# Kernel optimization log

Hardware: AMD Instinct MI355X
Metric: run time of the kernel (lower is better)

The kernel has to match this reference:

```python
import jax, jax.numpy as jnp
import numpy as np

HID = 1024            # hidden_dim
COND = 80             # cond_dim (mel bins)
EMB = HID // 8        # 128
D = HID // 4          # 256
NC = 2 ** 8           # num_coarse_bits = 8
NF = 2 ** 8           # num_fine_bits = 8
N, L = 32, 1024


def _vs(key, shape):
    # VarianceScaling(1.0, fan_in, truncated_normal) approximated by normal/sqrt(fan_in)
    return jax.random.normal(key, shape, jnp.float32) / jnp.sqrt(jnp.float32(shape[0]))


def setup_inputs() -> dict:
    key = jax.random.key(0)
    ks = jax.random.split(key, 16)
    x = jax.random.randint(ks[0], (N, L, 2), 0, NC, dtype=jnp.int64)
    mel = jax.random.normal(ks[1], (N, L, COND), jnp.float32)
    return {
        "x": x,
        "mel": mel,
        "R_w": _vs(ks[2], (HID, 3 * HID)),
        "R_b": jnp.zeros((3 * HID,), jnp.float32),
        "I_W": _vs(ks[3], (COND + 3 * EMB, 3 * HID)),
        "I_b": jnp.zeros((1, 3 * HID), jnp.float32),
        "O1_w": _vs(ks[4], (3 * D, 3 * D)),
        "O1_b": jnp.zeros((3 * D,), jnp.float32),
        "O2_w": _vs(ks[5], (3 * D, NC)),
        "O2_b": jnp.zeros((NC,), jnp.float32),
        "O3_w": _vs(ks[6], (D, D)),
        "O3_b": jnp.zeros((D,), jnp.float32),
        "O4_w": _vs(ks[7], (D, NF)),
        "O4_b": jnp.zeros((NF,), jnp.float32),
        "c_emb": jax.random.normal(ks[8], (NC, EMB), jnp.float32) * 0.02,
        "f_emb": jax.random.normal(ks[9], (NF, EMB), jnp.float32) * 0.02,
    }


def _mask_like(I_W):
    # zero out future-coarse embedding rows for the coarse-prediction gate halves
    m = jnp.ones_like(I_W)
    m = m.at[-EMB:, 0 * D:3 * D].set(0.0)
    m = m.at[-EMB:, 4 * D:7 * D].set(0.0)
    m = m.at[-EMB:, 8 * D:11 * D].set(0.0)
    return m


def _forward(x, mel, R_w, R_b, I_W, I_b, O1_w, O1_b, O2_w, O2_b, O3_w, O3_b, O4_w, O4_b, c_emb, f_emb):
    c = x[..., 0]
    f = x[..., 1]
    c_next = jnp.roll(c, -1, -1)
    # [N, L, COND + 3*EMB]
    inp = jnp.concatenate((mel, c_emb[c], f_emb[f], c_emb[c_next]), axis=-1)
    IW = I_W * _mask_like(I_W)
    # input projection is time-independent -> precompute for all steps: [N, L, 3H]
    xproj = jnp.einsum("nld,dh->nlh", inp, IW) + I_b[0]

    def step(h, xt):
        u1, r1, e1 = jnp.split(h @ R_w + R_b, 3, axis=-1)
        u2, r2, e2 = jnp.split(xt, 3, axis=-1)
        u = jax.nn.sigmoid(u1 + u2)
        r = jax.nn.sigmoid(r1 + r2)
        e = jnp.tanh(r * e1 + e2)
        h = u * h + (1.0 - u) * e
        return h, h

    h0 = jnp.zeros((x.shape[0], HID), xproj.dtype)
    _, hs = jax.lax.scan(step, h0, jnp.swapaxes(xproj, 0, 1))  # [L, N, H]
    hs = jnp.swapaxes(hs, 0, 1)                                 # [N, L, H]
    yc = hs[..., : 3 * D]
    yf = hs[..., 3 * D:]
    clogits = jax.nn.relu(yc @ O1_w + O1_b) @ O2_w + O2_b
    flogits = jax.nn.relu(yf @ O3_w + O3_b) @ O4_w + O4_b
    return clogits, flogits


def reference(x, mel, R_w, R_b, I_W, I_b, O1_w, O1_b, O2_w, O2_b, O3_w, O3_b, O4_w, O4_b, c_emb, f_emb):
    return _forward(x, mel, R_w, R_b, I_W, I_b, O1_w, O1_b, O2_w, O2_b,
                    O3_w, O3_b, O4_w, O4_b, c_emb, f_emb)
```

## Files before the change

### kernel.cpp

```cpp
#include <hip/hip_runtime.h>
#include <hip/hip_bf16.h>
#include <math.h>

typedef __attribute__((ext_vector_type(4))) float vf4;
typedef __attribute__((ext_vector_type(8))) short vbf8;
typedef __attribute__((ext_vector_type(8))) unsigned short vus8;

#define NWG   128
#define NTHR  256
#define LEN   1024
#define H3    3072
#define CND   80
#define EMBD  128

#define TAB1_B  0ull
#define TAB2_B  (TAB1_B + 786432ull*4)
#define TAB3_B  (TAB2_B + 786432ull*4)
#define BF_B    (TAB3_B + 786432ull*4)
#define MELA_B  (BF_B   + 4587520ull*2)
#define AF_B    (MELA_B + 3145728ull*2)
#define CNT_B   (AF_B   + 33587200ull*2)
#define W1F_B   (CNT_B + 4096ull)
#define W2F_B   (W1F_B + 1179648ull)
#define W3F_B   (W2F_B + 393216ull)
#define W4F_B   (W3F_B + 131072ull)
#define FOFS    8388608ull


__global__ __launch_bounds__(256) void make_tables(const float* __restrict__ IW,
                                                   const float* __restrict__ Ib,
                                                   const float* __restrict__ cemb,
                                                   const float* __restrict__ femb,
                                                   float* __restrict__ tab1,
                                                   float* __restrict__ tab2,
                                                   float* __restrict__ tab3) {
    int blk = blockIdx.x;
    int table = blk / 3072;
    int rem = blk % 3072;
    int row = rem / 12;
    int cc = rem % 12;
    int col = cc * 256 + threadIdx.x;
    int ofs = CND + table * EMBD;
    const float* emb = (table == 1) ? femb : cemb;
    float acc = 0.f;
    for (int k = 0; k < EMBD; ++k)
        acc += emb[row * EMBD + k] * IW[(size_t)(ofs + k) * H3 + col];
    if (table == 0) acc += Ib[col];
    if (table == 2 && ((col & 1023) < 768)) acc = 0.f;
    float* dst = (table == 0) ? tab1 : (table == 1 ? tab2 : tab3);
    dst[(size_t)row * H3 + col] = acc;
}

__global__ __launch_bounds__(256) void build_bfrag2(const float* __restrict__ Rw,
                                                    const float* __restrict__ IW,
                                                    const float* __restrict__ Rb,
                                                    unsigned short* __restrict__ Bf) {
    int idx = blockIdx.x * 256 + threadIdx.x;
    int col = idx % 3072;
    int k   = idx / 3072;
    float v;
    if (k < 1024)       v = Rw[(size_t)k * H3 + col];
    else if (k < 1104)  v = IW[(size_t)(k - 1024) * H3 + col];
    else if (k == 1104) v = Rb[col];
    else return;

    int g  = col >> 10;
    int j  = col & 1023;
    int oct = j >> 3, jo = j & 7;
    int which, c;
    if (g < 2)      { which = 0; c = g * 8 + jo; }
    else {
        which = 1;
        if (k < 1024 || k == 1104) c = jo;
        else                        c = 8 + jo;
    }
    int kk = k >> 5, r5 = k & 31;
    int lane = (r5 >> 3) * 16 + c;
    int elem = r5 & 7;
    size_t dst = (((size_t)oct * 2 + which) * 35 + kk) * 512 + lane * 8 + elem;
    __hip_bfloat16 hb = __float2bfloat16(v);
    Bf[dst] = *(unsigned short*)&hb;
}

__global__ __launch_bounds__(256) void build_melA(const float* __restrict__ mel,
                                                  unsigned short* __restrict__ MelA) {
    long idx = (long)blockIdx.x * 256 + threadIdx.x;
    int elem = idx & 7;
    int lane = (idx >> 3) & 63;
    int kkm  = (int)((idx >> 9) % 3);
    int m    = (int)((idx / 1536) & 1);
    int t    = (int)(idx / 3072);
    int b    = m * 16 + (lane & 15);
    int km   = kkm * 32 + ((lane >> 4) & 3) * 8 + elem;
    float v = (km < CND) ? mel[((size_t)b * LEN + t) * CND + km] : (km == CND ? 1.f : 0.f);
    __hip_bfloat16 hb = __float2bfloat16(v);
    MelA[idx] = *(unsigned short*)&hb;
}

__global__ __launch_bounds__(256) void build_wfrag(const float* __restrict__ W,
                                                   unsigned short* __restrict__ Wf,
                                                   int K, int N) {
    int idx = blockIdx.x * 256 + threadIdx.x;
    if (idx >= K * N) return;
    int col = idx % N;
    int k   = idx / N;
    int nt = col >> 4, c = col & 15;
    int kf = k >> 5, k5 = k & 31;
    int lane = c + 16 * (k5 >> 3);
    int elem = k5 & 7;
    size_t dst = ((size_t)nt * (K >> 5) + kf) * 512 + (size_t)lane * 8 + elem;
    __hip_bfloat16 hb = __float2bfloat16(W[idx]);
    Wf[dst] = *(unsigned short*)&hb;
}

__device__ __forceinline__ int is_sent(unsigned long long q) {
    return ((unsigned)q == 0xFFFFFFFFu) || ((unsigned)(q >> 32) == 0xFFFFFFFFu);
}

__global__ __launch_bounds__(256, 1) void scan_persist(const unsigned short* __restrict__ Bf,
                                                       const unsigned short* __restrict__ MelA,
                                                       unsigned short* __restrict__ Af,
                                                       const float* __restrict__ tab1,
                                                       const float* __restrict__ tab2,
                                                       const float* __restrict__ tab3,
                                                       const int* __restrict__ xin) {
    __shared__ __align__(16) unsigned short hstage[32 * 512];
    __shared__ float ex[16][68];

    int tid = threadIdx.x;
    int wg  = blockIdx.x;
    int lane = tid & 63;
    int wv = tid >> 6;
    int bh = wg >> 6;
    int jg = wg & 63;
    int p  = wv >> 1;
    int which = wv & 1;
    int oct = jg * 2 + p;

    vbf8 Breg[35];
    {
        const unsigned short* Bp = Bf + (((size_t)oct * 2 + which) * 35) * 512 + lane * 8;
#pragma unroll
        for (int kk = 0; kk < 35; ++kk)
            Breg[kk] = *(const vbf8*)(Bp + kk * 512);
    }

    int bl = tid >> 4, gjl = tid & 15;
    int gb = bh * 16 + bl;
    int gj = jg * 16 + gjl;
    float hreg = 0.f;
    size_t wbase = (size_t)((bh * 32 + (gj >> 5)) * 512 +
                            (bl + 16 * ((gj >> 3) & 3)) * 8 + (gj & 7));

#pragma unroll 1
    for (int t = 0; t < LEN; ++t) {
        int ci = xin[(gb * LEN + t) * 2];
        int fi = xin[(gb * LEN + t) * 2 + 1];
        int cn = xin[(gb * LEN + ((t + 1) & (LEN - 1))) * 2];
        float t1u = tab1[(size_t)ci * H3 + gj];
        float t2u = tab2[(size_t)fi * H3 + gj];
        float t3u = tab3[(size_t)cn * H3 + gj];
        float t1r = tab1[(size_t)ci * H3 + 1024 + gj];
        float t2r = tab2[(size_t)fi * H3 + 1024 + gj];
        float t3r = tab3[(size_t)cn * H3 + 1024 + gj];
        float t1e = tab1[(size_t)ci * H3 + 2048 + gj];
        float t2e = tab2[(size_t)fi * H3 + 2048 + gj];
        float t3e = tab3[(size_t)cn * H3 + 2048 + gj];

        int f0 = wv * 8;
        const unsigned long long* bp =
            (const unsigned long long*)(Af + (size_t)t * 32768 +
                                        (size_t)(bh * 32 + f0) * 512) + lane * 2;
        unsigned long long q[16];
#pragma unroll
        for (int i = 0; i < 8; ++i) {
            q[2 * i]     = __hip_atomic_load(bp + i * 128,     __ATOMIC_RELAXED, __HIP_MEMORY_SCOPE_AGENT);
            q[2 * i + 1] = __hip_atomic_load(bp + i * 128 + 1, __ATOMIC_RELAXED, __HIP_MEMORY_SCOPE_AGENT);
        }
        for (;;) {
            int bad = 0;
#pragma unroll
            for (int i = 0; i < 16; ++i) bad |= is_sent(q[i]);
            if (!__any(bad)) break;
            __builtin_amdgcn_s_sleep(1);
#pragma unroll
            for (int i = 0; i < 8; ++i) {
                q[2 * i]     = __hip_atomic_load(bp + i * 128,     __ATOMIC_RELAXED, __HIP_MEMORY_SCOPE_AGENT);
                q[2 * i + 1] = __hip_atomic_load(bp + i * 128 + 1, __ATOMIC_RELAXED, __HIP_MEMORY_SCOPE_AGENT);
            }
        }
#pragma unroll
        for (int i = 0; i < 8; ++i) {
            union { unsigned long long qq[2]; vus8 v; } u;
            u.qq[0] = q[2 * i]; u.qq[1] = q[2 * i + 1];
            *(vus8*)(hstage + (size_t)(f0 + i) * 512 + lane * 8) = u.v;
        }
        __syncthreads();

        const unsigned short* Am = MelA + (size_t)t * 3072 + (size_t)(bh * 3) * 512 + lane * 8;
        vf4 acc0 = {0.f, 0.f, 0.f, 0.f}, acc1 = {0.f, 0.f, 0.f, 0.f};
#pragma unroll
        for (int kq = 0; kq < 3; ++kq) {
            vbf8 a = *(const vbf8*)(Am + kq * 512);
            acc0 = __builtin_amdgcn_mfma_f32_16x16x32_bf16(a, Breg[32 + kq], acc0, 0, 0, 0);
        }

        const unsigned short* Ah = hstage + lane * 8;
#pragma unroll
        for (int kk = 0; kk < 32; kk += 2) {
            vbf8 a0v = *(const vbf8*)(Ah + kk * 512);
            acc0 = __builtin_amdgcn_mfma_f32_16x16x32_bf16(a0v, Breg[kk], acc0, 0, 0, 0);
            vbf8 a1v = *(const vbf8*)(Ah + (kk + 1) * 512);
            acc1 = __builtin_amdgcn_mfma_f32_16x16x32_bf16(a1v, Breg[kk + 1], acc1, 0, 0, 0);
        }
        vf4 acc = acc0 + acc1;

#pragma unroll
        for (int r = 0; r < 4; ++r)
            ex[(lane >> 4) * 4 + r][wv * 16 + (lane & 15)] = acc[r];
        __syncthreads();

        int pp = gjl >> 3, jo = gjl & 7;
        float gu  = ex[bl][(pp * 2) * 16 + jo]          + t1u + t2u + t3u;
        float gr  = ex[bl][(pp * 2) * 16 + 8 + jo]      + t1r + t2r + t3r;
        float e1  = ex[bl][(pp * 2 + 1) * 16 + jo];
        float ge2 = ex[bl][(pp * 2 + 1) * 16 + 8 + jo]  + t1e + t2e + t3e;
        float u  = 1.f / (1.f + expf(-gu));
        float r_ = 1.f / (1.f + expf(-gr));
        float e  = tanhf(r_ * e1 + ge2);
        hreg = u * hreg + (1.f - u) * e;

        __hip_bfloat16 hb = __float2bfloat16(hreg);
        int myv = (int)(*(unsigned short*)&hb);
        int nbv = __shfl_xor(myv, 1);
        if ((tid & 1) == 0) {
            unsigned int pk = ((unsigned)myv & 0xffffu) | ((unsigned)nbv << 16);
            __hip_atomic_store((unsigned int*)(Af + (size_t)(t + 1) * 32768 + wbase), pk,
                               __ATOMIC_RELAXED, __HIP_MEMORY_SCOPE_AGENT);
        }
        __syncthreads();
    }
}

__global__ __launch_bounds__(512) void out_mlp_mfma(
        const unsigned short* __restrict__ Af,
        const unsigned short* __restrict__ W1f, const float* __restrict__ O1b,
        const unsigned short* __restrict__ W2f, const float* __restrict__ O2b,
        const unsigned short* __restrict__ W3f, const float* __restrict__ O3b,
        const unsigned short* __restrict__ W4f, const float* __restrict__ O4b,
        float* __restrict__ out) {
    __shared__ __align__(16) unsigned short Zc[2 * 24 * 512];
    __shared__ __align__(16) unsigned short Zf[2 * 8 * 512];

    int tid = threadIdx.x;
    int lane = tid & 63;
    int wv = tid >> 6;
    int m = wv >> 2;
    int q = wv & 3;
    int l = blockIdx.x;
    int c16 = lane & 15;
    int rowq = lane >> 4;

    const unsigned short* Abase = Af + (size_t)(l + 1) * 32768 +
                                  (size_t)(m * 32) * 512 + (size_t)lane * 8;

    {
        vf4 acc[12];
#pragma unroll
        for (int i = 0; i < 12; ++i) acc[i] = (vf4){0.f, 0.f, 0.f, 0.f};
        for (int kk = 0; kk < 24; ++kk) {
            vbf8 a = *(const vbf8*)(Abase + kk * 512);
#pragma unroll
            for (int i = 0; i < 12; ++i) {
                int nt = q * 12 + i;
                vbf8 b = *(const vbf8*)(W1f + ((size_t)nt * 24 + kk) * 512 + lane * 8);
                acc[i] = __builtin_amdgcn_mfma_f32_16x16x32_bf16(a, b, acc[i], 0, 0, 0);
            }
        }
#pragma unroll
        for (int i = 0; i < 12; ++i) {
            int nt = q * 12 + i;
            int col = nt * 16 + c16;
            float bias = O1b[col];
#pragma unroll
            for (int r = 0; r < 4; ++r) {
                float v = fmaxf(acc[i][r] + bias, 0.f);
                __hip_bfloat16 hb = __float2bfloat16(v);
                int my = (int)*(unsigned short*)&hb;
                int nb = __shfl_xor(my, 1);
                if ((lane & 1) == 0) {
                    unsigned pk = ((unsigned)my & 0xffffu) | ((unsigned)nb << 16);
                    int row = rowq * 4 + r;
                    int kk2 = col >> 5, k5 = col & 31;
                    int lp = row + 16 * (k5 >> 3);
                    int ep = k5 & 7;
                    *(unsigned*)&Zc[(size_t)(m * 24 + kk2) * 512 + lp * 8 + ep] = pk;
                }
            }
        }
    }
    __syncthreads();

    {
        vf4 acc[4];
#pragma unroll
        for (int i = 0; i < 4; ++i) acc[i] = (vf4){0.f, 0.f, 0.f, 0.f};
        for (int kk = 0; kk < 24; ++kk) {
            vbf8 a = *(const vbf8*)(Zc + (size_t)(m * 24 + kk) * 512 + lane * 8);
#pragma unroll
            for (int i = 0; i < 4; ++i) {
                int nt = q * 4 + i;
                vbf8 b = *(const vbf8*)(W2f + ((size_t)nt * 24 + kk) * 512 + lane * 8);
                acc[i] = __builtin_amdgcn_mfma_f32_16x16x32_bf16(a, b, acc[i], 0, 0, 0);
            }
        }
#pragma unroll
        for (int i = 0; i < 4; ++i) {
            int nt = q * 4 + i;
            int col = nt * 16 + c16;
            float bias = O2b[col];
#pragma unroll
            for (int r = 0; r < 4; ++r) {
                int nn = m * 16 + rowq * 4 + r;
                out[((size_t)nn * 1024 + l) * 256 + col] = acc[i][r] + bias;
            }
        }
    }

    {
        vf4 acc[4];
#pragma unroll
        for (int i = 0; i < 4; ++i) acc[i] = (vf4){0.f, 0.f, 0.f, 0.f};
        for (int kf = 0; kf < 8; ++kf) {
            vbf8 a = *(const vbf8*)(Abase + (24 + kf) * 512);
#pragma unroll
            for (int i = 0; i < 4; ++i) {
                int nt = q * 4 + i;
                vbf8 b = *(const vbf8*)(W3f + ((size_t)nt * 8 + kf) * 512 + lane * 8);
                acc[i] = __builtin_amdgcn_mfma_f32_16x16x32_bf16(a, b, acc[i], 0, 0, 0);
            }
        }
#pragma unroll
        for (int i = 0; i < 4; ++i) {
            int nt = q * 4 + i;
            int col = nt * 16 + c16;
            float bias = O3b[col];
#pragma unroll
            for (int r = 0; r < 4; ++r) {
                float v = fmaxf(acc[i][r] + bias, 0.f);
                __hip_bfloat16 hb = __float2bfloat16(v);
                int my = (int)*(unsigned short*)&hb;
                int nb = __shfl_xor(my, 1);
                if ((lane & 1) == 0) {
                    unsigned pk = ((unsigned)my & 0xffffu) | ((unsigned)nb << 16);
                    int row = rowq * 4 + r;
                    int kk2 = col >> 5, k5 = col & 31;
                    int lp = row + 16 * (k5 >> 3);
                    int ep = k5 & 7;
                    *(unsigned*)&Zf[(size_t)(m * 8 + kk2) * 512 + lp * 8 + ep] = pk;
                }
            }
        }
    }
    __syncthreads();

    {
        vf4 acc[4];
#pragma unroll
        for (int i = 0; i < 4; ++i) acc[i] = (vf4){0.f, 0.f, 0.f, 0.f};
        for (int kf = 0; kf < 8; ++kf) {
            vbf8 a = *(const vbf8*)(Zf + (size_t)(m * 8 + kf) * 512 + lane * 8);
#pragma unroll
            for (int i = 0; i < 4; ++i) {
                int nt = q * 4 + i;
                vbf8 b = *(const vbf8*)(W4f + ((size_t)nt * 8 + kf) * 512 + lane * 8);
                acc[i] = __builtin_amdgcn_mfma_f32_16x16x32_bf16(a, b, acc[i], 0, 0, 0);
            }
        }
#pragma unroll
        for (int i = 0; i < 4; ++i) {
            int nt = q * 4 + i;
            int col = nt * 16 + c16;
            float bias = O4b[col];
#pragma unroll
            for (int r = 0; r < 4; ++r) {
                int nn = m * 16 + rowq * 4 + r;
                out[FOFS + ((size_t)nn * 1024 + l) * 256 + col] = acc[i][r] + bias;
            }
        }
    }
}

extern "C" void kernel_launch(void* const* d_in, const int* in_sizes, int n_in,
                              void* d_out, int out_size, void* d_ws, size_t ws_size,
                              hipStream_t stream) {
    const int*   x    = (const int*)d_in[0];
    const float* mel  = (const float*)d_in[1];
    const float* Rw   = (const float*)d_in[2];
    const float* Rb   = (const float*)d_in[3];
    const float* IW   = (const float*)d_in[4];
    const float* Ib   = (const float*)d_in[5];
    const float* O1w  = (const float*)d_in[6];
    const float* O1b  = (const float*)d_in[7];
    const float* O2w  = (const float*)d_in[8];
    const float* O2b  = (const float*)d_in[9];
    const float* O3w  = (const float*)d_in[10];
    const float* O3b  = (const float*)d_in[11];
    const float* O4w  = (const float*)d_in[12];
    const float* O4b  = (const float*)d_in[13];
    const float* cemb = (const float*)d_in[14];
    const float* femb = (const float*)d_in[15];
    char* wsb = (char*)d_ws;
    float* out = (float*)d_out;

    float* tab1 = (float*)(wsb + TAB1_B);
    float* tab2 = (float*)(wsb + TAB2_B);
    float* tab3 = (float*)(wsb + TAB3_B);
    unsigned short* Bf   = (unsigned short*)(wsb + BF_B);
    unsigned short* MelA = (unsigned short*)(wsb + MELA_B);
    unsigned short* Af   = (unsigned short*)(wsb + AF_B);
    unsigned short* W1f  = (unsigned short*)(wsb + W1F_B);
    unsigned short* W2f  = (unsigned short*)(wsb + W2F_B);
    unsigned short* W3f  = (unsigned short*)(wsb + W3F_B);
    unsigned short* W4f  = (unsigned short*)(wsb + W4F_B);

    make_tables<<<9216, 256, 0, stream>>>(IW, Ib, cemb, femb, tab1, tab2, tab3);
    hipMemsetAsync((void*)Bf, 0, 4587520ull * 2, stream);
    build_bfrag2<<<13440, 256, 0, stream>>>(Rw, IW, Rb, Bf);
    build_melA<<<12288, 256, 0, stream>>>(mel, MelA);
    build_wfrag<<<2304, 256, 0, stream>>>(O1w, W1f, 768, 768);
    build_wfrag<<<768,  256, 0, stream>>>(O2w, W2f, 768, 256);
    build_wfrag<<<256,  256, 0, stream>>>(O3w, W3f, 256, 256);
    build_wfrag<<<256,  256, 0, stream>>>(O4w, W4f, 256, 256);
    hipMemsetAsync((void*)Af, 0xFF, 33587200ull * 2, stream);
    hipMemsetAsync((void*)Af, 0, 65536, stream);

    scan_persist<<<NWG, NTHR, 0, stream>>>(Bf, MelA, Af, tab1, tab2, tab3, x);

    out_mlp_mfma<<<1024, 512, 0, stream>>>(Af, W1f, O1b, W2f, O2b, W3f, O3b, W4f, O4b, out);
}
```

Measured before the change: 2.873 ms.

## Split recurrent matmul by K across waves and reduce partials in LDS

```diff
diff --git a/kernel.cpp b/kernel.cpp
--- a/kernel.cpp
+++ b/kernel.cpp
@@ -124,8 +124,7 @@
                                                        const float* __restrict__ tab2,
                                                        const float* __restrict__ tab3,
                                                        const int* __restrict__ xin) {
-    __shared__ __align__(16) unsigned short hstage[32 * 512];
-    __shared__ float ex[16][68];
+    __shared__ float pex[4][4][256];
 
     int tid = threadIdx.x;
     int wg  = blockIdx.x;
@@ -133,17 +132,11 @@
     int wv = tid >> 6;
     int bh = wg >> 6;
     int jg = wg & 63;
-    int p  = wv >> 1;
-    int which = wv & 1;
-    int oct = jg * 2 + p;
-
-    vbf8 Breg[35];
-    {
-        const unsigned short* Bp = Bf + (((size_t)oct * 2 + which) * 35) * 512 + lane * 8;
-#pragma unroll
-        for (int kk = 0; kk < 35; ++kk)
-            Breg[kk] = *(const vbf8*)(Bp + kk * 512);
-    }
+
+    const unsigned short* Bp0 = Bf + (((size_t)(jg * 2 + 0) * 2 + 0) * 35) * 512 + lane * 8;
+    const unsigned short* Bp1 = Bf + (((size_t)(jg * 2 + 0) * 2 + 1) * 35) * 512 + lane * 8;
+    const unsigned short* Bp2 = Bf + (((size_t)(jg * 2 + 1) * 2 + 0) * 35) * 512 + lane * 8;
+    const unsigned short* Bp3 = Bf + (((size_t)(jg * 2 + 1) * 2 + 1) * 35) * 512 + lane * 8;
 
     int bl = tid >> 4, gjl = tid & 15;
     int gb = bh * 16 + bl;
@@ -151,6 +144,10 @@
     float hreg = 0.f;
     size_t wbase = (size_t)((bh * 32 + (gj >> 5)) * 512 +
                             (bl + 16 * ((gj >> 3) & 3)) * 8 + (gj & 7));
+    int p  = gjl >> 3, jo = gjl & 7;
+    int nt_ur = p * 2, nt_e = p * 2 + 1;
+    int ru = ((bl >> 2) * 16 + jo) * 4 + (bl & 3);
+    int rr = ((bl >> 2) * 16 + 8 + jo) * 4 + (bl & 3);
 
 #pragma unroll 1
     for (int t = 0; t < LEN; ++t) {
@@ -167,10 +164,9 @@
         float t2e = tab2[(size_t)fi * H3 + 2048 + gj];
         float t3e = tab3[(size_t)cn * H3 + 2048 + gj];
 
-        int f0 = wv * 8;
         const unsigned long long* bp =
             (const unsigned long long*)(Af + (size_t)t * 32768 +
-                                        (size_t)(bh * 32 + f0) * 512) + lane * 2;
+                                        (size_t)(bh * 32 + wv * 8) * 512) + lane * 2;
         unsigned long long q[16];
 #pragma unroll
         for (int i = 0; i < 8; ++i) {
@@ -189,42 +185,41 @@
                 q[2 * i + 1] = __hip_atomic_load(bp + i * 128 + 1, __ATOMIC_RELAXED, __HIP_MEMORY_SCOPE_AGENT);
             }
         }
+
+        vf4 acc0 = {0.f, 0.f, 0.f, 0.f}, acc1 = {0.f, 0.f, 0.f, 0.f};
+        vf4 acc2 = {0.f, 0.f, 0.f, 0.f}, acc3 = {0.f, 0.f, 0.f, 0.f};
 #pragma unroll
         for (int i = 0; i < 8; ++i) {
-            union { unsigned long long qq[2]; vus8 v; } u;
-            u.qq[0] = q[2 * i]; u.qq[1] = q[2 * i + 1];
-            *(vus8*)(hstage + (size_t)(f0 + i) * 512 + lane * 8) = u.v;
-        }
+            union { unsigned long long qq[2]; vbf8 v; } ua;
+            ua.qq[0] = q[2 * i]; ua.qq[1] = q[2 * i + 1];
+            vbf8 a = ua.v;
+            int kk = wv * 8 + i;
+            acc0 = __builtin_amdgcn_mfma_f32_16x16x32_bf16(a, *(const vbf8*)(Bp0 + kk * 512), acc0, 0, 0, 0);
+            acc1 = __builtin_amdgcn_mfma_f32_16x16x32_bf16(a, *(const vbf8*)(Bp1 + kk * 512), acc1, 0, 0, 0);
+            acc2 = __builtin_amdgcn_mfma_f32_16x16x32_bf16(a, *(const vbf8*)(Bp2 + kk * 512), acc2, 0, 0, 0);
+            acc3 = __builtin_amdgcn_mfma_f32_16x16x32_bf16(a, *(const vbf8*)(Bp3 + kk * 512), acc3, 0, 0, 0);
+        }
+        if (wv < 3) {
+            vbf8 am = *(const vbf8*)(MelA + (size_t)t * 3072 + (size_t)(bh * 3 + wv) * 512 + lane * 8);
+            acc0 = __builtin_amdgcn_mfma_f32_16x16x32_bf16(am, *(const vbf8*)(Bp0 + (32 + wv) * 512), acc0, 0, 0, 0);
+            acc1 = __builtin_amdgcn_mfma_f32_16x16x32_bf16(am, *(const vbf8*)(Bp1 + (32 + wv) * 512), acc1, 0, 0, 0);
+            acc2 = __builtin_amdgcn_mfma_f32_16x16x32_bf16(am, *(const vbf8*)(Bp2 + (32 + wv) * 512), acc2, 0, 0, 0);
+            acc3 = __builtin_amdgcn_mfma_f32_16x16x32_bf16(am, *(const vbf8*)(Bp3 + (32 + wv) * 512), acc3, 0, 0, 0);
+        }
+
+        *(vf4*)&pex[wv][0][lane * 4] = acc0;
+        *(vf4*)&pex[wv][1][lane * 4] = acc1;
+        *(vf4*)&pex[wv][2][lane * 4] = acc2;
+        *(vf4*)&pex[wv][3][lane * 4] = acc3;
         __syncthreads();
 
-        const unsigned short* Am = MelA + (size_t)t * 3072 + (size_t)(bh * 3) * 512 + lane * 8;
-        vf4 acc0 = {0.f, 0.f, 0.f, 0.f}, acc1 = {0.f, 0.f, 0.f, 0.f};
-#pragma unroll
-        for (int kq = 0; kq < 3; ++kq) {
-            vbf8 a = *(const vbf8*)(Am + kq * 512);
-            acc0 = __builtin_amdgcn_mfma_f32_16x16x32_bf16(a, Breg[32 + kq], acc0, 0, 0, 0);
-        }
-
-        const unsigned short* Ah = hstage + lane * 8;
-#pragma unroll
-        for (int kk = 0; kk < 32; kk += 2) {
-            vbf8 a0v = *(const vbf8*)(Ah + kk * 512);
-            acc0 = __builtin_amdgcn_mfma_f32_16x16x32_bf16(a0v, Breg[kk], acc0, 0, 0, 0);
-            vbf8 a1v = *(const vbf8*)(Ah + (kk + 1) * 512);
-            acc1 = __builtin_amdgcn_mfma_f32_16x16x32_bf16(a1v, Breg[kk + 1], acc1, 0, 0, 0);
-        }
-        vf4 acc = acc0 + acc1;
-
-#pragma unroll
-        for (int r = 0; r < 4; ++r)
-            ex[(lane >> 4) * 4 + r][wv * 16 + (lane & 15)] = acc[r];
-        __syncthreads();
-
-        int pp = gjl >> 3, jo = gjl & 7;
-        float gu  = ex[bl][(pp * 2) * 16 + jo]          + t1u + t2u + t3u;
-        float gr  = ex[bl][(pp * 2) * 16 + 8 + jo]      + t1r + t2r + t3r;
-        float e1  = ex[bl][(pp * 2 + 1) * 16 + jo];
-        float ge2 = ex[bl][(pp * 2 + 1) * 16 + 8 + jo]  + t1e + t2e + t3e;
+        float gu  = pex[0][nt_ur][ru] + pex[1][nt_ur][ru] + pex[2][nt_ur][ru] + pex[3][nt_ur][ru]
+                  + t1u + t2u + t3u;
+        float gr  = pex[0][nt_ur][rr] + pex[1][nt_ur][rr] + pex[2][nt_ur][rr] + pex[3][nt_ur][rr]
+                  + t1r + t2r + t3r;
+        float e1  = pex[0][nt_e][ru] + pex[1][nt_e][ru] + pex[2][nt_e][ru] + pex[3][nt_e][ru];
+        float ge2 = pex[0][nt_e][rr] + pex[1][nt_e][rr] + pex[2][nt_e][rr] + pex[3][nt_e][rr]
+                  + t1e + t2e + t3e;
         float u  = 1.f / (1.f + expf(-gu));
         float r_ = 1.f / (1.f + expf(-gr));
         float e  = tanhf(r_ * e1 + ge2);
```

After: 2.702 ms (median of 2 runs). -5.9%, faster.
